# Performance work log

Hardware: AMD Instinct MI355X
Metric: run time of the kernel (lower is better)

The kernel has to match this reference:

```python
import jax, jax.numpy as jnp
import numpy as np

DIM = 1024
HEADS = 16
DIM_HEAD = 64
B, N = 4, 2048


def setup_inputs() -> dict:
    key = jax.random.key(0)
    ks = jax.random.split(key, 10)
    s = 0.02
    x = jax.random.normal(ks[0], (B, N, DIM), dtype=jnp.float32)
    Wq = jax.random.normal(ks[1], (DIM, DIM), dtype=jnp.float32) * s
    bq = jnp.zeros((DIM,), dtype=jnp.float32)
    Wk = jax.random.normal(ks[2], (DIM, DIM), dtype=jnp.float32) * s
    bk = jnp.zeros((DIM,), dtype=jnp.float32)
    Wv = jax.random.normal(ks[3], (DIM, DIM), dtype=jnp.float32) * s
    bv = jnp.zeros((DIM,), dtype=jnp.float32)
    Wo = jax.random.normal(ks[4], (DIM, DIM), dtype=jnp.float32) * s
    bo = jnp.zeros((DIM,), dtype=jnp.float32)
    # learnable log-temperature, init = log(dim_head ** -0.5)
    log_temp = jnp.array(np.log(DIM_HEAD ** -0.5), dtype=jnp.float32)
    return {"x": x, "Wq": Wq, "bq": bq, "Wk": Wk, "bk": bk,
            "Wv": Wv, "bv": bv, "Wo": Wo, "bo": bo, "log_temp": log_temp}


def reference(x, Wq, bq, Wk, bk, Wv, bv, Wo, bo, log_temp):
    b, n, _ = x.shape
    # projections (dropout is identity at p=0)
    q = x @ Wq + bq
    k = x @ Wk + bk
    v = x @ Wv + bv
    # [b, n, h*d] -> [b, h, n, d]
    def split_heads(t):
        return t.reshape(b, n, HEADS, DIM_HEAD).transpose(0, 2, 1, 3)
    q, k, v = split_heads(q), split_heads(k), split_heads(v)
    # scaled dot-product scores with learnable temperature
    dots = jnp.einsum('bhid,bhjd->bhij', q, k) * jnp.exp(log_temp)
    # mask out self-attention (diagonal) with -finfo.max
    mask_value = -jnp.finfo(dots.dtype).max
    eye = jnp.eye(n, dtype=bool)
    dots = jnp.where(eye, mask_value, dots)
    attn = jax.nn.softmax(dots, axis=-1)
    out = jnp.einsum('bhij,bhjd->bhid', attn, v)
    # [b, h, n, d] -> [b, n, h*d]
    out = out.transpose(0, 2, 1, 3).reshape(b, n, HEADS * DIM_HEAD)
    return out @ Wo + bo
```

## Files before the change

kernel.cpp:

```cpp
#include <hip/hip_runtime.h>
#include <cmath>

typedef __bf16 bf16_t;
typedef __attribute__((ext_vector_type(8))) __bf16 bf16x8;
typedef __attribute__((ext_vector_type(4))) __bf16 bf16x4;
typedef __attribute__((ext_vector_type(4))) float f32x4;

#define SEQ   2048
#define NHEAD 16
#define DHEAD 64
#define NB    4
#define DIMSZ 1024
#define MROWS 8192

__device__ __forceinline__ void async_copy16(const void* g, void* lds) {
  __builtin_amdgcn_global_load_lds(
      (__attribute__((address_space(1))) void*)(g),
      (__attribute__((address_space(3))) void*)(lds), 16, 0, 0);
}

__device__ __forceinline__ f32x4 f32x4_zero() {
  f32x4 v; v[0] = 0.f; v[1] = 0.f; v[2] = 0.f; v[3] = 0.f; return v;
}

__global__ __launch_bounds__(256) void cvt_x(const float* __restrict__ x,
                                             bf16_t* __restrict__ xb) {
  size_t i = ((size_t)blockIdx.x * 256 + threadIdx.x) * 8;
  float4 f0 = *(const float4*)(x + i);
  float4 f1 = *(const float4*)(x + i + 4);
  bf16x8 o;
  o[0] = (__bf16)f0.x; o[1] = (__bf16)f0.y; o[2] = (__bf16)f0.z; o[3] = (__bf16)f0.w;
  o[4] = (__bf16)f1.x; o[5] = (__bf16)f1.y; o[6] = (__bf16)f1.z; o[7] = (__bf16)f1.w;
  *(bf16x8*)(xb + i) = o;
}

__global__ __launch_bounds__(256) void transpose_w(
    const float* __restrict__ W0, const float* __restrict__ W1,
    const float* __restrict__ W2, const float* __restrict__ W3,
    bf16_t* __restrict__ T0, bf16_t* __restrict__ T1,
    bf16_t* __restrict__ T2, bf16_t* __restrict__ T3) {
  const float* W; bf16_t* T;
  switch (blockIdx.z) {
    case 0: W = W0; T = T0; break;
    case 1: W = W1; T = T1; break;
    case 2: W = W2; T = T2; break;
    default: W = W3; T = T3; break;
  }
  __shared__ float t[32][33];
  int tx = threadIdx.x, ty = threadIdx.y;
  int col = blockIdx.x * 32 + tx;
#pragma unroll
  for (int i = 0; i < 4; i++) {
    int row = blockIdx.y * 32 + ty + i * 8;
    t[ty + i * 8][tx] = W[row * DIMSZ + col];
  }
  __syncthreads();
#pragma unroll
  for (int i = 0; i < 4; i++) {
    int n = blockIdx.x * 32 + ty + i * 8;
    int k = blockIdx.y * 32 + tx;
    T[n * DIMSZ + k] = (bf16_t)t[tx][ty + i * 8];
  }
}

__device__ __forceinline__ void gemm_mainloop(
    const bf16_t* __restrict__ A, const bf16_t* __restrict__ Bt,
    int m0, int n0, f32x4 acc[4][4]) {
  __shared__ __attribute__((aligned(16))) bf16_t As[2][128 * 64];
  __shared__ __attribute__((aligned(16))) bf16_t Bs[2][128 * 64];
  const int tid = threadIdx.x;
  const int wid = tid >> 6, lane = tid & 63;
  const int quad = lane >> 4, l16 = lane & 15;
  const int wm = wid & 1, wn = wid >> 1;
  const int srow = lane >> 3;
  const int gchunk = (lane & 7) ^ srow;
#pragma unroll
  for (int r = 0; r < 4; r++)
#pragma unroll
    for (int c = 0; c < 4; c++) acc[r][c] = f32x4_zero();

  const bf16_t* ag = A + (size_t)(m0 + wid * 8 + srow) * DIMSZ + gchunk * 8;
  const bf16_t* bg = Bt + (size_t)(n0 + wid * 8 + srow) * DIMSZ + gchunk * 8;

  auto stage = [&](int k0, int buf) {
#pragma unroll
    for (int c2 = 0; c2 < 4; c2++) {
      async_copy16(ag + (size_t)c2 * 32 * DIMSZ + k0, &As[buf][(c2 * 32 + wid * 8) * 64]);
      async_copy16(bg + (size_t)c2 * 32 * DIMSZ + k0, &Bs[buf][(c2 * 32 + wid * 8) * 64]);
    }
  };

  stage(0, 0);
  for (int it = 0; it < 16; it++) {
    const int p = it & 1;
    __syncthreads();
    if (it < 15) stage((it + 1) * 64, 1 - p);
#pragma unroll
    for (int kk = 0; kk < 2; kk++) {
      bf16x8 af[4], bfr[4];
#pragma unroll
      for (int r = 0; r < 4; r++) {
        int row = wm * 64 + r * 16 + l16;
        int slot = (kk * 4 + quad) ^ (row & 7);
        af[r] = *(const bf16x8*)(&As[p][0] + row * 64 + slot * 8);
      }
#pragma unroll
      for (int c = 0; c < 4; c++) {
        int row = wn * 64 + c * 16 + l16;
        int slot = (kk * 4 + quad) ^ (row & 7);
        bfr[c] = *(const bf16x8*)(&Bs[p][0] + row * 64 + slot * 8);
      }
#pragma unroll
      for (int r = 0; r < 4; r++)
#pragma unroll
        for (int c = 0; c < 4; c++)
          acc[r][c] = __builtin_amdgcn_mfma_f32_16x16x32_bf16(af[r], bfr[c],
                                                              acc[r][c], 0, 0, 0);
    }
  }
}

__global__ __launch_bounds__(256, 2) void gemm_qkv(
    const bf16_t* __restrict__ A,
    const bf16_t* __restrict__ Wt0, const bf16_t* __restrict__ Wt1,
    const bf16_t* __restrict__ Wt2,
    const float* __restrict__ b0, const float* __restrict__ b1,
    const float* __restrict__ b2,
    bf16_t* __restrict__ o0, bf16_t* __restrict__ o1, bf16_t* __restrict__ o2) {
  const bf16_t* Bt; const float* bias; bf16_t* dst;
  if (blockIdx.z == 0)      { Bt = Wt0; bias = b0; dst = o0; }
  else if (blockIdx.z == 1) { Bt = Wt1; bias = b1; dst = o1; }
  else                      { Bt = Wt2; bias = b2; dst = o2; }
  const int m0 = blockIdx.x * 128, n0 = blockIdx.y * 128;
  f32x4 acc[4][4];
  gemm_mainloop(A, Bt, m0, n0, acc);
  const int lane = threadIdx.x & 63, wid = threadIdx.x >> 6;
  const int quad = lane >> 4, l16 = lane & 15;
  const int wm = wid & 1, wn = wid >> 1;
  if (blockIdx.z == 2) {
#pragma unroll
    for (int c = 0; c < 4; c++) {
      int col = n0 + wn * 64 + c * 16 + l16;
      float bv = bias[col];
      int hh = col >> 6, dd = col & 63;
#pragma unroll
      for (int r = 0; r < 4; r++) {
        int row = m0 + wm * 64 + r * 16 + quad * 4;
        int bb = row >> 11, nn = row & (SEQ - 1);
        bf16x4 pk;
#pragma unroll
        for (int rr = 0; rr < 4; rr++) pk[rr] = (__bf16)(acc[r][c][rr] + bv);
        *(bf16x4*)(dst + ((size_t)(bb * NHEAD + hh) * DHEAD + dd) * SEQ + nn) = pk;
      }
    }
  } else {
#pragma unroll
    for (int c = 0; c < 4; c++) {
      int col = n0 + wn * 64 + c * 16 + l16;
      float bv = bias[col];
      int hh = col >> 6, dd = col & 63;
#pragma unroll
      for (int r = 0; r < 4; r++)
#pragma unroll
        for (int rr = 0; rr < 4; rr++) {
          int row = m0 + wm * 64 + r * 16 + quad * 4 + rr;
          int bb = row >> 11, nn = row & (SEQ - 1);
          dst[(((size_t)(bb * NHEAD + hh) * SEQ + nn) << 6) + dd] =
              (bf16_t)(acc[r][c][rr] + bv);
        }
    }
  }
}

__global__ __launch_bounds__(256, 2) void gemm_out(
    const bf16_t* __restrict__ A, const bf16_t* __restrict__ Bt,
    const float* __restrict__ bias, float* __restrict__ dst) {
  const int m0 = blockIdx.x * 128, n0 = blockIdx.y * 128;
  f32x4 acc[4][4];
  gemm_mainloop(A, Bt, m0, n0, acc);
  const int lane = threadIdx.x & 63, wid = threadIdx.x >> 6;
  const int quad = lane >> 4, l16 = lane & 15;
  const int wm = wid & 1, wn = wid >> 1;
#pragma unroll
  for (int c = 0; c < 4; c++) {
    int col = n0 + wn * 64 + c * 16 + l16;
    float bv = bias[col];
#pragma unroll
    for (int r = 0; r < 4; r++)
#pragma unroll
      for (int rr = 0; rr < 4; rr++) {
        int row = m0 + wm * 64 + r * 16 + quad * 4 + rr;
        dst[(size_t)row * DIMSZ + col] = acc[r][c][rr] + bv;
      }
  }
}

__global__ __launch_bounds__(256, 3) void attn_kernel(
    const bf16_t* __restrict__ qh, const bf16_t* __restrict__ kh,
    const bf16_t* __restrict__ vt, bf16_t* __restrict__ ao,
    const float* __restrict__ log_temp) {
  __shared__ __attribute__((aligned(16))) bf16_t Ks[2][64 * 64];
  __shared__ __attribute__((aligned(16))) bf16_t Vs[2][64 * 64];
  __shared__ __attribute__((aligned(16))) bf16_t Ps[4][32 * 64];
  const int tid = threadIdx.x;
  const int wid = tid >> 6, lane = tid & 63;
  const int quad = lane >> 4, l16 = lane & 15;
  const int i0 = blockIdx.x * 128;
  const int h = blockIdx.y, b = blockIdx.z;
  const size_t ho = (size_t)(b * NHEAD + h) * SEQ * DHEAD;
  const bf16_t* Q = qh + ho;
  const float ascale = expf(log_temp[0]) * 1.44269504f;
  const float bshift = 16.0f * 1.44269504f;

  const int irow = i0 + wid * 32;
  bf16x8 qf[2][2];
#pragma unroll
  for (int g = 0; g < 2; g++)
#pragma unroll
    for (int jj = 0; jj < 2; jj++)
      qf[g][jj] = *(const bf16x8*)(Q + (size_t)(irow + g * 16 + l16) * DHEAD +
                                   jj * 32 + quad * 8);

  f32x4 oacc[4][2];
#pragma unroll
  for (int c = 0; c < 4; c++)
#pragma unroll
    for (int g = 0; g < 2; g++) oacc[c][g] = f32x4_zero();
  float lsum[2] = {0.f, 0.f};

  const int srow = lane >> 3;
  const int gch = (lane & 7) ^ srow;
  const bf16_t* kg = kh + ho + (size_t)(wid * 8 + srow) * DHEAD + gch * 8;
  const bf16_t* vg = vt + ho + (size_t)(wid * 8 + srow) * SEQ + gch * 8;
  bf16_t* Pw = Ps[wid];
  const int x7 = l16 & 7;
  const int jdiag_t = blockIdx.x * 2 + (wid >> 1);

  int kvoff[4][2];
#pragma unroll
  for (int c = 0; c < 4; c++)
#pragma unroll
    for (int kk = 0; kk < 2; kk++) {
      int row = c * 16 + l16;
      kvoff[c][kk] = row * 64 + (((kk * 4) + quad) ^ x7) * 8;
    }
  bf16_t* pwa[2][4];
#pragma unroll
  for (int g = 0; g < 2; g++)
#pragma unroll
    for (int c = 0; c < 4; c++) {
      int slot = (2 * c + (quad >> 1)) ^ x7;
      pwa[g][c] = Pw + (g * 16 + l16) * 64 + slot * 8 + (quad & 1) * 4;
    }
  const bf16_t* paa[2][2];
#pragma unroll
  for (int g = 0; g < 2; g++)
#pragma unroll
    for (int kk = 0; kk < 2; kk++)
      paa[g][kk] = Pw + (g * 16 + l16) * 64 + (((kk * 4) + quad) ^ x7) * 8;

  auto stage = [&](int jt, int buf) {
    const bf16_t* kp = kg + (size_t)jt * 64 * DHEAD;
    const bf16_t* vp = vg + jt * 64;
    bf16_t* kd = &Ks[buf][wid * 8 * 64];
    bf16_t* vd = &Vs[buf][wid * 8 * 64];
    async_copy16(kp, kd);
    async_copy16(kp + 32 * DHEAD, kd + 32 * 64);
    async_copy16(vp, vd);
    async_copy16(vp + 32 * SEQ, vd + 32 * 64);
  };

  stage(0, 0);
  for (int jt = 0; jt < SEQ / 64; jt++) {
    const int p = jt & 1;
    __syncthreads();
    if (jt + 1 < SEQ / 64) stage(jt + 1, 1 - p);
    const bf16_t* Kp = &Ks[p][0];
    const bf16_t* Vp = &Vs[p][0];

    f32x4 st[4][2];
#pragma unroll
    for (int c = 0; c < 4; c++) {
      bf16x8 kf0 = *(const bf16x8*)(Kp + kvoff[c][0]);
      bf16x8 kf1 = *(const bf16x8*)(Kp + kvoff[c][1]);
#pragma unroll
      for (int g = 0; g < 2; g++) {
        f32x4 s = f32x4_zero();
        s = __builtin_amdgcn_mfma_f32_16x16x32_bf16(kf0, qf[g][0], s, 0, 0, 0);
        s = __builtin_amdgcn_mfma_f32_16x16x32_bf16(kf1, qf[g][1], s, 0, 0, 0);
        st[c][g] = s;
      }
    }

    const int j0 = jt * 64;
    if (jt == jdiag_t) {
#pragma unroll
      for (int g = 0; g < 2; g++) {
        float ls = 0.f;
        const int ig = irow + g * 16 + l16;
#pragma unroll
        for (int c = 0; c < 4; c++) {
          bf16x4 pk;
#pragma unroll
          for (int rr = 0; rr < 4; rr++) {
            float e = __builtin_amdgcn_exp2f(fmaf(st[c][g][rr], ascale, -bshift));
            if (j0 + c * 16 + quad * 4 + rr == ig) e = 0.f;
            ls += e;
            pk[rr] = (__bf16)e;
          }
          *(bf16x4*)pwa[g][c] = pk;
        }
        lsum[g] += ls;
      }
    } else {
#pragma unroll
      for (int g = 0; g < 2; g++) {
        float ls = 0.f;
#pragma unroll
        for (int c = 0; c < 4; c++) {
          bf16x4 pk;
#pragma unroll
          for (int rr = 0; rr < 4; rr++) {
            float e = __builtin_amdgcn_exp2f(fmaf(st[c][g][rr], ascale, -bshift));
            ls += e;
            pk[rr] = (__bf16)e;
          }
          *(bf16x4*)pwa[g][c] = pk;
        }
        lsum[g] += ls;
      }
    }

    bf16x8 pa[2][2];
#pragma unroll
    for (int g = 0; g < 2; g++) {
      pa[g][0] = *(const bf16x8*)paa[g][0];
      pa[g][1] = *(const bf16x8*)paa[g][1];
    }
#pragma unroll
    for (int c = 0; c < 4; c++) {
      bf16x8 vb0 = *(const bf16x8*)(Vp + kvoff[c][0]);
      bf16x8 vb1 = *(const bf16x8*)(Vp + kvoff[c][1]);
#pragma unroll
      for (int g = 0; g < 2; g++) {
        oacc[c][g] = __builtin_amdgcn_mfma_f32_16x16x32_bf16(pa[g][0], vb0,
                                                             oacc[c][g], 0, 0, 0);
        oacc[c][g] = __builtin_amdgcn_mfma_f32_16x16x32_bf16(pa[g][1], vb1,
                                                             oacc[c][g], 0, 0, 0);
      }
    }
  }

#pragma unroll
  for (int g = 0; g < 2; g++) {
    lsum[g] += __shfl_xor(lsum[g], 16);
    lsum[g] += __shfl_xor(lsum[g], 32);
  }
#pragma unroll
  for (int g = 0; g < 2; g++)
#pragma unroll
    for (int rr = 0; rr < 4; rr++) {
      float lr = __shfl(lsum[g], (lane & 48) | (quad * 4 + rr));
      float inv = 1.f / lr;
      int row = irow + g * 16 + quad * 4 + rr;
#pragma unroll
      for (int c = 0; c < 4; c++) {
        ao[(size_t)(b * SEQ + row) * DIMSZ + h * DHEAD + c * 16 + l16] =
            (bf16_t)(oacc[c][g][rr] * inv);
      }
    }
}

extern "C" void kernel_launch(void* const* d_in, const int* in_sizes, int n_in,
                              void* d_out, int out_size, void* d_ws, size_t ws_size,
                              hipStream_t stream) {
  const float* x  = (const float*)d_in[0];
  const float* Wq = (const float*)d_in[1];
  const float* bq = (const float*)d_in[2];
  const float* Wk = (const float*)d_in[3];
  const float* bk = (const float*)d_in[4];
  const float* Wv = (const float*)d_in[5];
  const float* bv = (const float*)d_in[6];
  const float* Wo = (const float*)d_in[7];
  const float* bo = (const float*)d_in[8];
  const float* lt = (const float*)d_in[9];

  bf16_t* xb  = (bf16_t*)d_ws;
  bf16_t* wtq = xb  + (size_t)MROWS * DIMSZ;
  bf16_t* wtk = wtq + (size_t)DIMSZ * DIMSZ;
  bf16_t* wtv = wtk + (size_t)DIMSZ * DIMSZ;
  bf16_t* wto = wtv + (size_t)DIMSZ * DIMSZ;
  bf16_t* qh  = wto + (size_t)DIMSZ * DIMSZ;
  bf16_t* kh  = qh  + (size_t)MROWS * DIMSZ;
  bf16_t* vh  = kh  + (size_t)MROWS * DIMSZ;
  bf16_t* ao  = xb;

  cvt_x<<<dim3(MROWS * DIMSZ / 2048), dim3(256), 0, stream>>>(x, xb);
  transpose_w<<<dim3(32, 32, 4), dim3(32, 8), 0, stream>>>(
      Wq, Wk, Wv, Wo, wtq, wtk, wtv, wto);
  gemm_qkv<<<dim3(64, 8, 3), dim3(256), 0, stream>>>(
      xb, wtq, wtk, wtv, bq, bk, bv, qh, kh, vh);
  attn_kernel<<<dim3(16, NHEAD, NB), dim3(256), 0, stream>>>(qh, kh, vh, ao, lt);
  gemm_out<<<dim3(64, 8), dim3(256), 0, stream>>>(ao, wto, bo, (float*)d_out);
}
```

Baseline: 279.6 us.

## Keep attention P in registers via permlane swaps instead of LDS round-trip

Removes the per-wave LDS buffer for softmax probabilities. Probabilities are now packed into bf16 pairs and redistributed across lanes with permlane32/16 swaps, and the PV MFMA is computed in transposed form (V as A operand), so the output accumulators hold rows per lane and can be written with vectorized bf16x4 stores. The change also flattens the grid so that heads and batches vary fastest across consecutive blocks, and raises the occupancy hint to 4 blocks per CU. It depends on the permlane swap instructions being available and carries correctness risk from the lane remapping.

```diff
diff --git a/kernel.cpp b/kernel.cpp
--- a/kernel.cpp
+++ b/kernel.cpp
@@ -4,7 +4,9 @@
 typedef __bf16 bf16_t;
 typedef __attribute__((ext_vector_type(8))) __bf16 bf16x8;
 typedef __attribute__((ext_vector_type(4))) __bf16 bf16x4;
+typedef __attribute__((ext_vector_type(2))) __bf16 bf16x2;
 typedef __attribute__((ext_vector_type(4))) float f32x4;
+typedef __attribute__((ext_vector_type(4))) unsigned uint4v;
 
 #define SEQ   2048
 #define NHEAD 16
@@ -21,6 +23,24 @@
 
 __device__ __forceinline__ f32x4 f32x4_zero() {
   f32x4 v; v[0] = 0.f; v[1] = 0.f; v[2] = 0.f; v[3] = 0.f; return v;
+}
+
+__device__ __forceinline__ void permlane_xform(unsigned& a, unsigned& b) {
+#if __has_builtin(__builtin_amdgcn_permlane32_swap) && __has_builtin(__builtin_amdgcn_permlane16_swap)
+  typedef __attribute__((ext_vector_type(2))) unsigned uint2v;
+  uint2v r1 = __builtin_amdgcn_permlane32_swap(a, b, false, false);
+  uint2v r2 = __builtin_amdgcn_permlane16_swap(r1[0], r1[1], false, false);
+  a = r2[0]; b = r2[1];
+#else
+  asm volatile("v_permlane32_swap_b32 %0, %1\n\t"
+               "v_permlane16_swap_b32 %0, %1"
+               : "+v"(a), "+v"(b));
+#endif
+}
+
+__device__ __forceinline__ unsigned pack_bf16(float lo, float hi) {
+  bf16x2 t; t[0] = (__bf16)lo; t[1] = (__bf16)hi;
+  return __builtin_bit_cast(unsigned, t);
 }
 
 __global__ __launch_bounds__(256) void cvt_x(const float* __restrict__ x,
@@ -195,18 +215,19 @@
   }
 }
 
-__global__ __launch_bounds__(256, 3) void attn_kernel(
+__global__ __launch_bounds__(256, 4) void attn_kernel(
     const bf16_t* __restrict__ qh, const bf16_t* __restrict__ kh,
     const bf16_t* __restrict__ vt, bf16_t* __restrict__ ao,
     const float* __restrict__ log_temp) {
   __shared__ __attribute__((aligned(16))) bf16_t Ks[2][64 * 64];
   __shared__ __attribute__((aligned(16))) bf16_t Vs[2][64 * 64];
-  __shared__ __attribute__((aligned(16))) bf16_t Ps[4][32 * 64];
   const int tid = threadIdx.x;
   const int wid = tid >> 6, lane = tid & 63;
   const int quad = lane >> 4, l16 = lane & 15;
-  const int i0 = blockIdx.x * 128;
-  const int h = blockIdx.y, b = blockIdx.z;
+  const int f = blockIdx.x;
+  const int hb = f & 63;
+  const int h = hb & 15, b = hb >> 4;
+  const int i0 = (f >> 6) * 128;
   const size_t ho = (size_t)(b * NHEAD + h) * SEQ * DHEAD;
   const bf16_t* Q = qh + ho;
   const float ascale = expf(log_temp[0]) * 1.44269504f;
@@ -221,43 +242,26 @@
       qf[g][jj] = *(const bf16x8*)(Q + (size_t)(irow + g * 16 + l16) * DHEAD +
                                    jj * 32 + quad * 8);
 
-  f32x4 oacc[4][2];
+  f32x4 oaccT[4][2];
 #pragma unroll
   for (int c = 0; c < 4; c++)
 #pragma unroll
-    for (int g = 0; g < 2; g++) oacc[c][g] = f32x4_zero();
+    for (int g = 0; g < 2; g++) oaccT[c][g] = f32x4_zero();
   float lsum[2] = {0.f, 0.f};
 
   const int srow = lane >> 3;
   const int gch = (lane & 7) ^ srow;
   const bf16_t* kg = kh + ho + (size_t)(wid * 8 + srow) * DHEAD + gch * 8;
   const bf16_t* vg = vt + ho + (size_t)(wid * 8 + srow) * SEQ + gch * 8;
-  bf16_t* Pw = Ps[wid];
   const int x7 = l16 & 7;
-  const int jdiag_t = blockIdx.x * 2 + (wid >> 1);
+  const int jdiag_t = (f >> 6) * 2 + (wid >> 1);
 
   int kvoff[4][2];
 #pragma unroll
   for (int c = 0; c < 4; c++)
 #pragma unroll
-    for (int kk = 0; kk < 2; kk++) {
-      int row = c * 16 + l16;
-      kvoff[c][kk] = row * 64 + (((kk * 4) + quad) ^ x7) * 8;
-    }
-  bf16_t* pwa[2][4];
-#pragma unroll
-  for (int g = 0; g < 2; g++)
-#pragma unroll
-    for (int c = 0; c < 4; c++) {
-      int slot = (2 * c + (quad >> 1)) ^ x7;
-      pwa[g][c] = Pw + (g * 16 + l16) * 64 + slot * 8 + (quad & 1) * 4;
-    }
-  const bf16_t* paa[2][2];
-#pragma unroll
-  for (int g = 0; g < 2; g++)
-#pragma unroll
     for (int kk = 0; kk < 2; kk++)
-      paa[g][kk] = Pw + (g * 16 + l16) * 64 + (((kk * 4) + quad) ^ x7) * 8;
+      kvoff[c][kk] = (c * 16 + l16) * 64 + (((kk * 4) + quad) ^ x7) * 8;
 
   auto stage = [&](int jt, int buf) {
     const bf16_t* kp = kg + (size_t)jt * 64 * DHEAD;
@@ -293,6 +297,7 @@
     }
 
     const int j0 = jt * 64;
+    unsigned pkv[2][4][2];
     if (jt == jdiag_t) {
 #pragma unroll
       for (int g = 0; g < 2; g++) {
@@ -300,15 +305,16 @@
         const int ig = irow + g * 16 + l16;
 #pragma unroll
         for (int c = 0; c < 4; c++) {
-          bf16x4 pk;
+          float e[4];
 #pragma unroll
           for (int rr = 0; rr < 4; rr++) {
-            float e = __builtin_amdgcn_exp2f(fmaf(st[c][g][rr], ascale, -bshift));
-            if (j0 + c * 16 + quad * 4 + rr == ig) e = 0.f;
-            ls += e;
-            pk[rr] = (__bf16)e;
+            float v = __builtin_amdgcn_exp2f(fmaf(st[c][g][rr], ascale, -bshift));
+            if (j0 + c * 16 + quad * 4 + rr == ig) v = 0.f;
+            e[rr] = v;
           }
-          *(bf16x4*)pwa[g][c] = pk;
+          ls += (e[0] + e[1]) + (e[2] + e[3]);
+          pkv[g][c][0] = pack_bf16(e[0], e[1]);
+          pkv[g][c][1] = pack_bf16(e[2], e[3]);
         }
         lsum[g] += ls;
       }
@@ -318,35 +324,42 @@
         float ls = 0.f;
 #pragma unroll
         for (int c = 0; c < 4; c++) {
-          bf16x4 pk;
-#pragma unroll
-          for (int rr = 0; rr < 4; rr++) {
-            float e = __builtin_amdgcn_exp2f(fmaf(st[c][g][rr], ascale, -bshift));
-            ls += e;
-            pk[rr] = (__bf16)e;
-          }
-          *(bf16x4*)pwa[g][c] = pk;
+          float e[4];
+#pragma unroll
+          for (int rr = 0; rr < 4; rr++)
+            e[rr] = __builtin_amdgcn_exp2f(fmaf(st[c][g][rr], ascale, -bshift));
+          ls += (e[0] + e[1]) + (e[2] + e[3]);
+          pkv[g][c][0] = pack_bf16(e[0], e[1]);
+          pkv[g][c][1] = pack_bf16(e[2], e[3]);
         }
         lsum[g] += ls;
       }
     }
 
-    bf16x8 pa[2][2];
+    bf16x8 pb[2][2];
 #pragma unroll
     for (int g = 0; g < 2; g++) {
-      pa[g][0] = *(const bf16x8*)paa[g][0];
-      pa[g][1] = *(const bf16x8*)paa[g][1];
-    }
+#pragma unroll
+      for (int kk = 0; kk < 2; kk++) {
+        unsigned a0 = pkv[g][2 * kk][0], b0 = pkv[g][2 * kk + 1][0];
+        unsigned a1 = pkv[g][2 * kk][1], b1 = pkv[g][2 * kk + 1][1];
+        permlane_xform(a0, b0);
+        permlane_xform(a1, b1);
+        uint4v u = {a0, a1, b0, b1};
+        pb[g][kk] = __builtin_bit_cast(bf16x8, u);
+      }
+    }
+
 #pragma unroll
     for (int c = 0; c < 4; c++) {
-      bf16x8 vb0 = *(const bf16x8*)(Vp + kvoff[c][0]);
-      bf16x8 vb1 = *(const bf16x8*)(Vp + kvoff[c][1]);
+      bf16x8 va0 = *(const bf16x8*)(Vp + kvoff[c][0]);
+      bf16x8 va1 = *(const bf16x8*)(Vp + kvoff[c][1]);
 #pragma unroll
       for (int g = 0; g < 2; g++) {
-        oacc[c][g] = __builtin_amdgcn_mfma_f32_16x16x32_bf16(pa[g][0], vb0,
-                                                             oacc[c][g], 0, 0, 0);
-        oacc[c][g] = __builtin_amdgcn_mfma_f32_16x16x32_bf16(pa[g][1], vb1,
-                                                             oacc[c][g], 0, 0, 0);
+        oaccT[c][g] = __builtin_amdgcn_mfma_f32_16x16x32_bf16(va0, pb[g][0],
+                                                              oaccT[c][g], 0, 0, 0);
+        oaccT[c][g] = __builtin_amdgcn_mfma_f32_16x16x32_bf16(va1, pb[g][1],
+                                                              oaccT[c][g], 0, 0, 0);
       }
     }
   }
@@ -355,20 +368,20 @@
   for (int g = 0; g < 2; g++) {
     lsum[g] += __shfl_xor(lsum[g], 16);
     lsum[g] += __shfl_xor(lsum[g], 32);
-  }
-#pragma unroll
-  for (int g = 0; g < 2; g++)
-#pragma unroll
-    for (int rr = 0; rr < 4; rr++) {
-      float lr = __shfl(lsum[g], (lane & 48) | (quad * 4 + rr));
-      float inv = 1.f / lr;
-      int row = irow + g * 16 + quad * 4 + rr;
-#pragma unroll
-      for (int c = 0; c < 4; c++) {
-        ao[(size_t)(b * SEQ + row) * DIMSZ + h * DHEAD + c * 16 + l16] =
-            (bf16_t)(oacc[c][g][rr] * inv);
-      }
-    }
+    lsum[g] = 1.f / lsum[g];
+  }
+#pragma unroll
+  for (int g = 0; g < 2; g++) {
+    const int row = irow + g * 16 + l16;
+#pragma unroll
+    for (int c = 0; c < 4; c++) {
+      bf16x4 o;
+#pragma unroll
+      for (int rr = 0; rr < 4; rr++) o[rr] = (__bf16)(oaccT[c][g][rr] * lsum[g]);
+      *(bf16x4*)(ao + (size_t)(b * SEQ + row) * DIMSZ + h * DHEAD + c * 16 +
+                 quad * 4) = o;
+    }
+  }
 }
 
 extern "C" void kernel_launch(void* const* d_in, const int* in_sizes, int n_in,
@@ -400,6 +413,6 @@
       Wq, Wk, Wv, Wo, wtq, wtk, wtv, wto);
   gemm_qkv<<<dim3(64, 8, 3), dim3(256), 0, stream>>>(
       xb, wtq, wtk, wtv, bq, bk, bv, qh, kh, vh);
-  attn_kernel<<<dim3(16, NHEAD, NB), dim3(256), 0, stream>>>(qh, kh, vh, ao, lt);
+  attn_kernel<<<dim3(16 * NHEAD * NB), dim3(256), 0, stream>>>(qh, kh, vh, ao, lt);
   gemm_out<<<dim3(64, 8), dim3(256), 0, stream>>>(ao, wto, bo, (float*)d_out);
 }
```

New measurement: 269.6 us. 1.04x faster.
